# Optimization experiments

Measured on AMD Instinct MI355X. Metric: run time of the kernel, lower is better.

The kernel has to match this reference:

```python
import jax, jax.numpy as jnp
import numpy as np

N_HEAD = 8
NORM_GROUPS = 32
EPS = 1e-6


def setup_inputs() -> dict:
    key = jax.random.key(0)
    ks = jax.random.split(key, 9)
    B, C, H, W, D = 1, 256, 16, 16, 16
    COND = 512
    x = jax.random.normal(ks[0], (B, C, H, W, D), dtype=jnp.float32)
    cond = jax.random.normal(ks[1], (B, COND), dtype=jnp.float32)
    # AdaGN linear scale/shift (torch Linear: weight [C, cond_dim], bias [C])
    w_scale = jax.random.normal(ks[2], (C, COND), dtype=jnp.float32) * 0.02
    b_scale = jax.random.normal(ks[3], (C,), dtype=jnp.float32) * 0.02
    w_shift = jax.random.normal(ks[4], (C, COND), dtype=jnp.float32) * 0.02
    b_shift = jax.random.normal(ks[5], (C,), dtype=jnp.float32) * 0.02
    # 1x1x1 conv3d weights collapse to matrices: qkv [3C, C] (no bias), out [C, C] + bias
    w_qkv = jax.random.normal(ks[6], (3 * C, C), dtype=jnp.float32) * (1.0 / np.sqrt(C))
    w_out = jax.random.normal(ks[7], (C, C), dtype=jnp.float32) * (1.0 / np.sqrt(C))
    b_out = jax.random.normal(ks[8], (C,), dtype=jnp.float32) * 0.02
    return {"x": x, "cond": cond, "w_scale": w_scale, "b_scale": b_scale,
            "w_shift": w_shift, "b_shift": b_shift, "w_qkv": w_qkv,
            "w_out": w_out, "b_out": b_out}


def _ada_gn(x, cond, w_scale, b_scale, w_shift, b_shift):
    B, C, H, W, D = x.shape
    G = NORM_GROUPS
    xg = x.reshape(B, G, C // G, H, W, D)
    mean = jnp.mean(xg, axis=(2, 3, 4, 5), keepdims=True)
    var = jnp.var(xg, axis=(2, 3, 4, 5), keepdims=True)
    x_norm = ((xg - mean) * jax.lax.rsqrt(var + EPS)).reshape(B, C, H, W, D)
    scale = (cond @ w_scale.T + b_scale)[:, :, None, None, None]  # [B,C,1,1,1]
    shift = (cond @ w_shift.T + b_shift)[:, :, None, None, None]
    return x_norm * (1.0 + scale) + shift


def reference(x, cond, w_scale, b_scale, w_shift, b_shift, w_qkv, w_out, b_out):
    B, C, H, W, D = x.shape
    nh = N_HEAD
    hd = C // nh
    N = H * W * D  # flattened spatial tokens
    norm = _ada_gn(x, cond, w_scale, b_scale, w_shift, b_shift)
    # 1x1x1 conv == channel matmul
    qkv = jnp.einsum('oc,bchwd->bohwd', w_qkv, norm)        # [B,3C,H,W,D]
    qkv = qkv.reshape(B, nh, 3 * hd, N)
    q, k, v = jnp.split(qkv, 3, axis=2)                      # each [B,nh,hd,N]
    attn = jnp.einsum('bnci,bncj->bnij', q, k) / jnp.sqrt(jnp.float32(C))
    attn = jax.nn.softmax(attn, axis=-1)                     # [B,nh,N,N]
    out = jnp.einsum('bnij,bncj->bnci', attn, v)             # [B,nh,hd,N]
    out = out.reshape(B, C, H, W, D)
    out = jnp.einsum('oc,bchwd->bohwd', w_out, out) + b_out[None, :, None, None, None]
    return out + x
```

## Files before the change

### kernel.cpp

```cpp
#include <hip/hip_runtime.h>
#include <math.h>

#define CCH 256
#define NN  4096
#define NHEAD 8
#define CONDD 512

typedef __attribute__((ext_vector_type(8))) short short8;
typedef __attribute__((ext_vector_type(4))) float f32x4;
typedef __attribute__((ext_vector_type(16))) float f32x16;

static __device__ __forceinline__ short f2bf(float f) {
    union { float f; uint32_t u; } v; v.f = f;
    uint32_t r = v.u + 0x7fffu + ((v.u >> 16) & 1u);
    return (short)(r >> 16);
}

static __device__ __forceinline__ uint32_t cvt_pk_bf16(float a, float b) {
    uint32_t r;
    asm("v_cvt_pk_bf16_f32 %0, %1, %2" : "=v"(r) : "v"(a), "v"(b));
    return r;
}

__global__ __launch_bounds__(256) void front_fused(const float* __restrict__ x,
                                                   const float* __restrict__ cond,
                                                   const float* __restrict__ w_scale,
                                                   const float* __restrict__ b_scale,
                                                   const float* __restrict__ w_shift,
                                                   const float* __restrict__ b_shift,
                                                   const float* __restrict__ wq,
                                                   const float* __restrict__ wo,
                                                   float* __restrict__ partial,
                                                   float* __restrict__ scale,
                                                   float* __restrict__ shift,
                                                   short* __restrict__ wqb,
                                                   short* __restrict__ wob) {
    __shared__ float rs[4], rss[4];
    int bb = blockIdx.x;
    int t = threadIdx.x;
    if (bb < 256) {
        const float4* p = (const float4*)(x + bb * 4096);
        float s = 0.f, ss = 0.f;
        for (int k = t; k < 1024; k += 256) {
            float4 v = p[k];
            s += v.x + v.y + v.z + v.w;
            ss += v.x * v.x + v.y * v.y + v.z * v.z + v.w * v.w;
        }
        #pragma unroll
        for (int off = 32; off; off >>= 1) { s += __shfl_xor(s, off); ss += __shfl_xor(ss, off); }
        int wid = t >> 6;
        if ((t & 63) == 0) { rs[wid] = s; rss[wid] = ss; }
        __syncthreads();
        if (t == 0) {
            partial[2 * bb] = rs[0] + rs[1] + rs[2] + rs[3];
            partial[2 * bb + 1] = rss[0] + rss[1] + rss[2] + rss[3];
        }
    } else if (bb < 1280) {
        int idx = (bb - 256) * 256 + t;
        if (idx < 196608) wqb[idx] = f2bf(wq[idx]);
        else              wob[idx - 196608] = f2bf(wo[idx - 196608]);
    } else {
        int o = (bb - 1280) * 4 + (t >> 6);
        int lane = t & 63;
        float ds = 0.f, dh = 0.f;
        for (int k = lane; k < CONDD; k += 64) {
            float cv = cond[k];
            ds += cv * w_scale[o * CONDD + k];
            dh += cv * w_shift[o * CONDD + k];
        }
        #pragma unroll
        for (int off = 32; off; off >>= 1) { ds += __shfl_xor(ds, off); dh += __shfl_xor(dh, off); }
        if (lane == 0) { scale[o] = ds + b_scale[o]; shift[o] = dh + b_shift[o]; }
    }
}

__global__ __launch_bounds__(256) void normalize_t(const float* __restrict__ x,
                                                   const float* __restrict__ partial,
                                                   const float* __restrict__ scale,
                                                   const float* __restrict__ shift,
                                                   short* __restrict__ norm_t) {
    __shared__ float gm[8], gr[8];
    __shared__ float Aa[64], Bb[64];
    __shared__ short tile[32 * 66];
    int i0 = blockIdx.x * 32;
    int c0 = blockIdx.y * 64;
    int g0 = c0 >> 3;
    int t = threadIdx.x;
    if (t < 8) {
        float s = 0.f, ss = 0.f;
        #pragma unroll
        for (int ch = 0; ch < 8; ++ch) {
            s += partial[((g0 + t) * 8 + ch) * 2];
            ss += partial[((g0 + t) * 8 + ch) * 2 + 1];
        }
        float mean = s * (1.0f / 32768.0f);
        float var = ss * (1.0f / 32768.0f) - mean * mean;
        gm[t] = mean;
        gr[t] = rsqrtf(var + 1e-6f);
    }
    __syncthreads();
    if (t < 64) {
        int c = c0 + t;
        float a = gr[t >> 3] * (1.0f + scale[c]);
        Aa[t] = a;
        Bb[t] = shift[c] - gm[t >> 3] * a;
    }
    __syncthreads();
    #pragma unroll
    for (int e0 = 0; e0 < 8; ++e0) {
        int e = e0 * 256 + t;
        int cl = e >> 5, il = e & 31;
        float v = x[(c0 + cl) * NN + i0 + il];
        tile[il * 66 + cl] = f2bf(v * Aa[cl] + Bb[cl]);
    }
    __syncthreads();
    #pragma unroll
    for (int e0 = 0; e0 < 4; ++e0) {
        int e = e0 * 256 + t;
        int il = e >> 5, cd = e & 31;
        uint32_t d = *(const uint32_t*)&tile[il * 66 + 2 * cd];
        *(uint32_t*)&norm_t[(i0 + il) * 256 + c0 + 2 * cd] = d;
    }
}

__global__ __launch_bounds__(256) void qkv_gemm(const short* __restrict__ wqb,
                                                const short* __restrict__ norm_t,
                                                short* __restrict__ qtb, short* __restrict__ ktb,
                                                short* __restrict__ vcb) {
    int t = threadIdx.x;
    int w = t >> 6, lane = t & 63, li = lane & 15, lg = lane >> 4;
    int o0 = blockIdx.x * 32;
    int i0 = blockIdx.y * 64 + w * 16;
    f32x4 acc[2] = {{0,0,0,0},{0,0,0,0}};
    const short* bbase = norm_t + (i0 + li) * 256 + 8 * lg;
    const short* abase = wqb + (o0 + li) * 256 + 8 * lg;
    #pragma unroll
    for (int ks = 0; ks < 8; ++ks) {
        short8 bfrag = *(const short8*)(bbase + ks * 32);
        #pragma unroll
        for (int f = 0; f < 2; ++f) {
            short8 afrag = *(const short8*)(abase + f * 16 * 256 + ks * 32);
            acc[f] = __builtin_amdgcn_mfma_f32_16x16x32_bf16(afrag, bfrag, acc[f], 0, 0, 0);
        }
    }
    int i = i0 + li;
    #pragma unroll
    for (int f = 0; f < 2; ++f) {
        #pragma unroll
        for (int r = 0; r < 4; ++r) {
            int o = o0 + 16 * f + 4 * lg + r;
            float v = acc[f][r];
            int h = o / 96;
            int rr = o - h * 96;
            int cc = rr & 31;
            int kind = rr >> 5;
            if (kind == 0)      qtb[(h * NN + i) * 32 + cc] = f2bf(v * (0.0625f * 1.44269504f));
            else if (kind == 1) ktb[(h * NN + i) * 32 + cc] = f2bf(v);
            else                vcb[(h * 32 + cc) * NN + i] = f2bf(v);
        }
    }
}

__global__ __launch_bounds__(512, 4) void attention_mfma(const short* __restrict__ qtb,
                                                         const short* __restrict__ ktb,
                                                         const short* __restrict__ vcb,
                                                         short* __restrict__ attnP,
                                                         float* __restrict__ plsum) {
    __shared__ __align__(16) char lds[49152];

    int bid = blockIdx.x;
    int h = bid & 7;
    int qb = (bid >> 3) & 15;
    int kh = bid >> 7;
    int t = threadIdx.x;
    int w = t >> 6, lane = t & 63, l31 = lane & 31, hi = lane >> 5;

    int qbase = qb * 256 + w * 32;
    const short* qrow = qtb + (h * NN + qbase + l31) * 32;
    short8 qf0 = *(const short8*)(qrow + 8 * hi);
    short8 qf1 = *(const short8*)(qrow + 16 + 8 * hi);
    asm volatile("s_waitcnt vmcnt(0)" ::: "memory");

    const char* src0;
    const char* src1;
    int ldsoff0, ldsoff1, step;
    if (w < 4) {
        int row_l = lane >> 2, g_lds = lane & 3;
        int g_glob = g_lds ^ (row_l & 3);
        const char* kbase = (const char*)ktb + (size_t)(h * NN + kh * 1024) * 64;
        int s0 = 2 * w, s1 = 2 * w + 1;
        src0 = kbase + ((s0 >> 2) * 64 + (s0 & 3) * 16 + row_l) * 64 + g_glob * 16;
        src1 = kbase + ((s1 >> 2) * 64 + (s1 & 3) * 16 + row_l) * 64 + g_glob * 16;
        ldsoff0 = s0 * 1024;
        ldsoff1 = s1 * 1024;
        step = 8192;
    } else {
        int row_l = lane >> 3, vs_lds = lane & 7;
        int vg = vs_lds ^ row_l;
        const char* vbase = (const char*)vcb + (size_t)(h * 32) * (NN * 2) + kh * 2048;
        int s0 = 2 * (w - 4), s1 = 2 * (w - 4) + 1;
        src0 = vbase + (size_t)((s0 & 3) * 8 + row_l) * (NN * 2) + (s0 >> 2) * 128 + vg * 16;
        src1 = vbase + (size_t)((s1 & 3) * 8 + row_l) * (NN * 2) + (s1 >> 2) * 128 + vg * 16;
        ldsoff0 = 8192 + s0 * 1024;
        ldsoff1 = 8192 + s1 * 1024;
        step = 256;
    }

    f32x16 acc = {0,0,0,0,0,0,0,0,0,0,0,0,0,0,0,0};
    const f32x16 zero16 = {0,0,0,0,0,0,0,0,0,0,0,0,0,0,0,0};
    float lsum = 0.f;

    #define ISSUE(st, b) do { \
        __builtin_amdgcn_global_load_lds((const uint32_t*)(src0 + (st) * step), \
            (uint32_t*)(lds + (b) * 16384 + ldsoff0), 16, 0, 0); \
        __builtin_amdgcn_global_load_lds((const uint32_t*)(src1 + (st) * step), \
            (uint32_t*)(lds + (b) * 16384 + ldsoff1), 16, 0, 0); \
    } while (0)

    #define COMPUTE(b) do { \
        const char* bb_ = lds + (b) * 16384; \
        _Pragma("unroll") \
        for (int chunk = 0; chunk < 2; ++chunk) { \
            _Pragma("unroll") \
            for (int half = 0; half < 2; ++half) { \
                int jl = half * 32; \
                int R = jl + l31; \
                int rx = R & 3; \
                const char* kr = bb_ + chunk * 4096 + R * 64; \
                short8 kf0 = *(const short8*)(kr + (((hi) ^ rx) << 4)); \
                short8 kf1 = *(const short8*)(kr + (((2 + hi) ^ rx) << 4)); \
                const char* vr = bb_ + 8192 + chunk * 4096 + l31 * 128; \
                int cx = l31 & 7; \
                int sv = (jl >> 3) + hi; \
                short8 vf0 = *(const short8*)(vr + ((sv ^ cx) << 4)); \
                short8 vf1 = *(const short8*)(vr + (((sv + 2) ^ cx) << 4)); \
                __builtin_amdgcn_s_setprio(1); \
                f32x16 s = __builtin_amdgcn_mfma_f32_32x32x16_bf16(kf0, qf0, zero16, 0, 0, 0); \
                s = __builtin_amdgcn_mfma_f32_32x32x16_bf16(kf1, qf1, s, 0, 0, 0); \
                __builtin_amdgcn_s_setprio(0); \
                float p[16]; \
                _Pragma("unroll") \
                for (int r = 0; r < 16; ++r) p[r] = __builtin_amdgcn_exp2f(s[r]); \
                float u0 = 0.f, u1 = 0.f; \
                _Pragma("unroll") \
                for (int r = 0; r < 4; ++r) { u0 += p[r] + p[4 + r]; u1 += p[8 + r] + p[12 + r]; } \
                lsum += u0 + u1; \
                auto A1 = __builtin_amdgcn_permlane32_swap(cvt_pk_bf16(p[0], p[1]),   cvt_pk_bf16(p[4], p[5]),   false, false); \
                auto A2 = __builtin_amdgcn_permlane32_swap(cvt_pk_bf16(p[2], p[3]),   cvt_pk_bf16(p[6], p[7]),   false, false); \
                auto A3 = __builtin_amdgcn_permlane32_swap(cvt_pk_bf16(p[8], p[9]),   cvt_pk_bf16(p[12], p[13]), false, false); \
                auto A4 = __builtin_amdgcn_permlane32_swap(cvt_pk_bf16(p[10], p[11]), cvt_pk_bf16(p[14], p[15]), false, false); \
                union PF { uint32_t u[4]; short8 s8; }; \
                PF f1, f2; \
                f1.u[0] = A1[0]; f1.u[1] = A2[0]; f1.u[2] = A1[1]; f1.u[3] = A2[1]; \
                f2.u[0] = A3[0]; f2.u[1] = A4[0]; f2.u[2] = A3[1]; f2.u[3] = A4[1]; \
                __builtin_amdgcn_s_setprio(1); \
                acc = __builtin_amdgcn_mfma_f32_32x32x16_bf16(vf0, f1.s8, acc, 0, 0, 0); \
                acc = __builtin_amdgcn_mfma_f32_32x32x16_bf16(vf1, f2.s8, acc, 0, 0, 0); \
                __builtin_amdgcn_s_setprio(0); \
            } \
        } \
    } while (0)

    ISSUE(0, 0);
    ISSUE(1, 1);
    ISSUE(2, 2);
    asm volatile("s_waitcnt vmcnt(4)" ::: "memory");
    __builtin_amdgcn_s_barrier();

    #pragma unroll
    for (int st = 0; st < 5; ++st) {
        COMPUTE(st % 3);
        __builtin_amdgcn_s_barrier();
        ISSUE(st + 3, st % 3);
        asm volatile("s_waitcnt vmcnt(4)" ::: "memory");
        __builtin_amdgcn_s_barrier();
    }
    COMPUTE(2);
    __builtin_amdgcn_s_barrier();
    asm volatile("s_waitcnt vmcnt(2)" ::: "memory");
    __builtin_amdgcn_s_barrier();
    COMPUTE(0);
    __builtin_amdgcn_s_barrier();
    asm volatile("s_waitcnt vmcnt(0)" ::: "memory");
    __builtin_amdgcn_s_barrier();
    COMPUTE(1);

    #undef ISSUE
    #undef COMPUTE

    __builtin_amdgcn_s_barrier();

    lsum += __shfl_xor(lsum, 32);

    short* tile = (short*)lds + w * 1024;
    #pragma unroll
    for (int g = 0; g < 4; ++g) {
        uint2 u;
        u.x = cvt_pk_bf16(acc[4 * g + 0], acc[4 * g + 1]);
        u.y = cvt_pk_bf16(acc[4 * g + 2], acc[4 * g + 3]);
        *(uint2*)(tile + l31 * 32 + 8 * g + 4 * hi) = u;
    }
    {
        int row = l31, half = hi;
        const uint4* srcp = (const uint4*)(tile + row * 32 + half * 16);
        short* dst = attnP + (size_t)(qbase + row) * 1024 + kh * 256 + h * 32 + half * 16;
        uint4 d0 = srcp[0];
        uint4 d1 = srcp[1];
        *(uint4*)dst = d0;
        *(uint4*)(dst + 8) = d1;
    }
    if (hi == 0) plsum[(size_t)(kh * 8 + h) * NN + qbase + l31] = lsum;
}

__global__ __launch_bounds__(256) void proj_gemm(const short* __restrict__ wob,
                                                 const short* __restrict__ attnP,
                                                 const float* __restrict__ plsum,
                                                 const float* __restrict__ b_out,
                                                 const float* __restrict__ x,
                                                 float* __restrict__ out) {
    __shared__ float invl[8][64];
    int t = threadIdx.x;
    int w = t >> 6, lane = t & 63, li = lane & 15, lg = lane >> 4;
    int o0 = blockIdx.x * 32;
    int i0b = blockIdx.y * 64;
    int i0 = i0b + w * 16;
    {
        int hh = t >> 5, ii = (t & 31) * 2;
        float a = 0.f, b = 0.f;
        #pragma unroll
        for (int kh = 0; kh < 4; ++kh) {
            const float* pl = plsum + (size_t)(kh * 8 + hh) * NN + i0b;
            a += pl[ii];
            b += pl[ii + 1];
        }
        invl[hh][ii] = 1.0f / a;
        invl[hh][ii + 1] = 1.0f / b;
    }
    __syncthreads();
    const short* bbase = attnP + (size_t)(i0 + li) * 1024 + 8 * lg;
    const short* abase = wob + (o0 + li) * 256 + 8 * lg;
    f32x4 facc0 = {0, 0, 0, 0}, facc1 = {0, 0, 0, 0};
    #pragma unroll
    for (int h = 0; h < 8; ++h) {
        short8 af0 = *(const short8*)(abase + h * 32);
        short8 af1 = *(const short8*)(abase + 16 * 256 + h * 32);
        f32x4 acc0 = {0, 0, 0, 0}, acc1 = {0, 0, 0, 0};
        #pragma unroll
        for (int kh = 0; kh < 4; ++kh) {
            short8 bf = *(const short8*)(bbase + kh * 256 + h * 32);
            acc0 = __builtin_amdgcn_mfma_f32_16x16x32_bf16(af0, bf, acc0, 0, 0, 0);
            acc1 = __builtin_amdgcn_mfma_f32_16x16x32_bf16(af1, bf, acc1, 0, 0, 0);
        }
        float iv = invl[h][w * 16 + li];
        facc0 += acc0 * iv;
        facc1 += acc1 * iv;
    }
    int i = i0 + li;
    #pragma unroll
    for (int r = 0; r < 4; ++r) {
        int o = o0 + 4 * lg + r;
        out[o * NN + i] = facc0[r] + b_out[o] + x[o * NN + i];
        int o2 = o0 + 16 + 4 * lg + r;
        out[o2 * NN + i] = facc1[r] + b_out[o2] + x[o2 * NN + i];
    }
}

extern "C" void kernel_launch(void* const* d_in, const int* in_sizes, int n_in,
                              void* d_out, int out_size, void* d_ws, size_t ws_size,
                              hipStream_t stream) {
    const float* x       = (const float*)d_in[0];
    const float* cond    = (const float*)d_in[1];
    const float* w_scale = (const float*)d_in[2];
    const float* b_scale = (const float*)d_in[3];
    const float* w_shift = (const float*)d_in[4];
    const float* b_shift = (const float*)d_in[5];
    const float* w_qkv   = (const float*)d_in[6];
    const float* w_out   = (const float*)d_in[7];
    const float* b_out   = (const float*)d_in[8];
    float* out = (float*)d_out;

    float* ws = (float*)d_ws;
    float* scale   = ws;
    float* shift   = ws + 256;
    float* partial = ws + 512;
    short* norm_t = (short*)(ws + 1024);
    short* qtb = norm_t + 1048576;
    short* ktb = qtb + 1048576;
    short* vcb = ktb + 1048576;
    short* wqb = vcb + 1048576;
    short* wob = wqb + 196608;
    short* attnP = wob + 65536;
    float* plsum = (float*)(attnP + (size_t)4096 * 1024);

    front_fused<<<1344, 256, 0, stream>>>(x, cond, w_scale, b_scale, w_shift, b_shift,
                                          w_qkv, w_out, partial, scale, shift, wqb, wob);
    normalize_t<<<dim3(128, 4), 256, 0, stream>>>(x, partial, scale, shift, norm_t);
    qkv_gemm<<<dim3(24, 64), 256, 0, stream>>>(wqb, norm_t, qtb, ktb, vcb);
    attention_mfma<<<512, 512, 0, stream>>>(qtb, ktb, vcb, attnP, plsum);
    proj_gemm<<<dim3(8, 64), 256, 0, stream>>>(wob, attnP, plsum, b_out, x, out);
}
```

Before: 73.56 us.

## Use four-stage LDS ring so loads issue before compute without extra barrier

Grows the attention kernel's LDS buffer from three to four stages and restructures the K/V pipeline so each next tile's global-to-LDS load is issued before computing the current stage. This removes one barrier per iteration and lets loads overlap compute longer. A sched_barrier is added to stop the compiler moving work across the wait. The cost is more LDS per block (64KB), which may reduce how many blocks fit per CU compared with the launch-bounds target of 4.

```diff
diff --git a/kernel.cpp b/kernel.cpp
--- a/kernel.cpp
+++ b/kernel.cpp
@@ -166,7 +166,7 @@
                                                          const short* __restrict__ vcb,
                                                          short* __restrict__ attnP,
                                                          float* __restrict__ plsum) {
-    __shared__ __align__(16) char lds[49152];
+    __shared__ __align__(16) char lds[65536];
 
     int bid = blockIdx.x;
     int h = bid & 7;
@@ -261,32 +261,29 @@
         } \
     } while (0)
 
+    #define WAITV(n) do { \
+        asm volatile("s_waitcnt vmcnt(" #n ")" ::: "memory"); \
+        __builtin_amdgcn_sched_barrier(0); \
+        __builtin_amdgcn_s_barrier(); \
+    } while (0)
+
     ISSUE(0, 0);
     ISSUE(1, 1);
     ISSUE(2, 2);
-    asm volatile("s_waitcnt vmcnt(4)" ::: "memory");
-    __builtin_amdgcn_s_barrier();
-
-    #pragma unroll
-    for (int st = 0; st < 5; ++st) {
-        COMPUTE(st % 3);
-        __builtin_amdgcn_s_barrier();
-        ISSUE(st + 3, st % 3);
-        asm volatile("s_waitcnt vmcnt(4)" ::: "memory");
-        __builtin_amdgcn_s_barrier();
-    }
-    COMPUTE(2);
-    __builtin_amdgcn_s_barrier();
-    asm volatile("s_waitcnt vmcnt(2)" ::: "memory");
-    __builtin_amdgcn_s_barrier();
-    COMPUTE(0);
-    __builtin_amdgcn_s_barrier();
-    asm volatile("s_waitcnt vmcnt(0)" ::: "memory");
-    __builtin_amdgcn_s_barrier();
-    COMPUTE(1);
+    WAITV(4);
+
+    ISSUE(3, 3); COMPUTE(0); WAITV(4);
+    ISSUE(4, 0); COMPUTE(1); WAITV(4);
+    ISSUE(5, 1); COMPUTE(2); WAITV(4);
+    ISSUE(6, 2); COMPUTE(3); WAITV(4);
+    ISSUE(7, 3); COMPUTE(0); WAITV(4);
+    COMPUTE(1); WAITV(2);
+    COMPUTE(2); WAITV(0);
+    COMPUTE(3);
 
     #undef ISSUE
     #undef COMPUTE
+    #undef WAITV
 
     __builtin_amdgcn_s_barrier();
 
```

Result: no change. 73.69 us (+0.2%).
